# Kernel tuning notes

Hardware: AMD Instinct MI355X
Metric: run time of the kernel (lower is better)

The kernel has to match this reference:

```python
import jax, jax.numpy as jnp
import numpy as np

DEPTH = 3  # weights are SHARED across depth (same module object repeated in ModuleList)


def prelu(x, a):
    # nn.PReLU() with a single shared slope parameter
    return jnp.where(x >= 0, x, a * x)


def conv1x1(x, w, b):
    # x: (N,C,H,W), w: (O,C), b: (O,)
    return jnp.einsum('nchw,oc->nohw', x, w) + b[None, :, None, None]


def conv3x3(x, w, b):
    # w: (O,I,3,3), padding=1 stride=1 -> SAME
    y = jax.lax.conv_general_dilated(x, w, (1, 1), 'SAME',
                                     dimension_numbers=('NCHW', 'OIHW', 'NCHW'))
    return y + b[None, :, None, None]


def _unit(x, w1, b1, a1, w2, b2, a2, w3, b3, a3, wc, bc):
    # NonLocalAttention
    e1 = prelu(conv1x1(x, w1, b1), a1)   # (N,C,H,W)
    e2 = prelu(conv1x1(x, w2, b2), a2)   # (N,C,H,W)
    asm = prelu(conv1x1(x, w3, b3), a3)  # (N,C,H,W)
    N, C, H, W = e1.shape
    q = e1.reshape(N, C, H * W).transpose(0, 2, 1)     # (N,HW,C)
    k = e2.reshape(N, C, H * W)                        # (N,C,HW)
    score = jax.nn.softmax(jnp.matmul(q, k), axis=2)   # (N,HW,HW)
    v = asm.reshape(N, C, H * W).transpose(0, 2, 1)    # (N,HW,C)
    att = jnp.matmul(score, v).transpose(0, 2, 1).reshape(N, C, H, W)
    # Conv2d(channel, channel, 3, 1, 1) + exact GELU
    return jax.nn.gelu(conv3x3(att, wc, bc), approximate=False)


def setup_inputs() -> dict:
    key = jax.random.key(0)
    ks = jax.random.split(key, 8)
    C = 128
    x = jax.random.normal(ks[0], (1, C, 96, 96), dtype=jnp.float32)
    s = 0.05
    inp = {
        'x': x,
        'w1': jax.random.normal(ks[1], (C, C), jnp.float32) * s,
        'b1': jnp.zeros((C,), jnp.float32),
        'a1': jnp.float32(0.25),
        'w2': jax.random.normal(ks[2], (C, C), jnp.float32) * s,
        'b2': jnp.zeros((C,), jnp.float32),
        'a2': jnp.float32(0.25),
        'w3': jax.random.normal(ks[3], (C, C), jnp.float32) * s,
        'b3': jnp.zeros((C,), jnp.float32),
        'a3': jnp.float32(0.25),
        'wc': jax.random.normal(ks[4], (C, C, 3, 3), jnp.float32) * s,
        'bc': jnp.zeros((C,), jnp.float32),
    }
    return inp


def reference(x, w1, b1, a1, w2, b2, a2, w3, b3, a3, wc, bc):
    res = x
    for _ in range(DEPTH):  # same (shared) weights each iteration, per original module
        res = _unit(res, w1, b1, a1, w2, b2, a2, w3, b3, a3, wc, bc)
    return x + res
```

## Files before the change

kernel.cpp:

```cpp
#include <hip/hip_runtime.h>

#define HWPX 9216
#define NCH  128

typedef float  f32x4  __attribute__((ext_vector_type(4)));
typedef __bf16 bf16x8 __attribute__((ext_vector_type(8)));

#define SWZ16(row) ((((row) & 7) ^ (((row) >> 3) << 1)) << 4)

#define DPP_RED(v, OP)                                                         \
  do {                                                                         \
    v = OP(v, __int_as_float(__builtin_amdgcn_update_dpp(                      \
               0, __float_as_int(v), 0xB1, 0xF, 0xF, true)));                  \
    v = OP(v, __int_as_float(__builtin_amdgcn_update_dpp(                      \
               0, __float_as_int(v), 0x4E, 0xF, 0xF, true)));                  \
    v = OP(v, __int_as_float(__builtin_amdgcn_update_dpp(                      \
               0, __float_as_int(v), 0x124, 0xF, 0xF, true)));                 \
    v = OP(v, __int_as_float(__builtin_amdgcn_update_dpp(                      \
               0, __float_as_int(v), 0x128, 0xF, 0xF, true)));                 \
  } while (0)
__device__ __forceinline__ float op_max(float a, float b) { return fmaxf(a, b); }
__device__ __forceinline__ float op_add(float a, float b) { return a + b; }

__global__ __launch_bounds__(256) void prep_kernel(
    const float* __restrict__ w1, const float* __restrict__ w2,
    const float* __restrict__ w3, const float* __restrict__ wc,
    const float* __restrict__ x,
    __bf16* __restrict__ Wb, __bf16* __restrict__ wck,
    __bf16* __restrict__ Xb) {
  int tid = blockIdx.x * 256 + threadIdx.x;
  int nt  = gridDim.x * 256;
  for (int idx = tid; idx < 3 * 16384; idx += nt) {
    int j = idx >> 14;
    const float* w = (j == 0) ? w1 : (j == 1 ? w2 : w3);
    Wb[idx] = (__bf16)w[idx & 16383];
  }
  for (int idx = tid; idx < 147456; idx += nt) {
    int k = idx % 9;
    int rest = idx / 9;
    int c = rest & 127, o = rest >> 7;
    wck[(k * 128 + o) * 128 + c] = (__bf16)wc[idx];
  }
  for (int idx = tid; idx < 128 * HWPX; idx += nt) {
    int c = idx / HWPX, p = idx - c * HWPX;
    Xb[p * 128 + c] = (__bf16)x[idx];
  }
}

__global__ __launch_bounds__(256) void conv1x1_qkv(
    const __bf16* __restrict__ Xb, const __bf16* __restrict__ Wb,
    const float* __restrict__ b1, const float* __restrict__ b2,
    const float* __restrict__ b3, const float* __restrict__ a1,
    const float* __restrict__ a2, const float* __restrict__ a3,
    __bf16* __restrict__ Q, __bf16* __restrict__ K, __bf16* __restrict__ Vt) {
  const int tid = threadIdx.x, lane = tid & 63, w = tid >> 6;
  const int l16 = lane & 15, hi = lane >> 4;
  const int p0 = blockIdx.x * 64;
  const int z  = blockIdx.y;

  bf16x8 af[4][4];
#pragma unroll
  for (int pxt = 0; pxt < 4; ++pxt)
#pragma unroll
    for (int kc = 0; kc < 4; ++kc)
      af[pxt][kc] = *(const bf16x8*)&Xb[(p0 + pxt * 16 + l16) * 128 + kc * 32 + hi * 8];

  const int obase = w * 96 + z * 16;
  const int j = obase >> 7;
  const int oo = (obase & 127) + l16;
  bf16x8 bfg[4];
#pragma unroll
  for (int kc = 0; kc < 4; ++kc)
    bfg[kc] = *(const bf16x8*)&Wb[(obase + l16) * 128 + kc * 32 + hi * 8];
  f32x4 acc[4];
#pragma unroll
  for (int pxt = 0; pxt < 4; ++pxt) acc[pxt] = (f32x4){0.f, 0.f, 0.f, 0.f};
#pragma unroll
  for (int kc = 0; kc < 4; ++kc)
#pragma unroll
    for (int pxt = 0; pxt < 4; ++pxt)
      acc[pxt] = __builtin_amdgcn_mfma_f32_16x16x32_bf16(af[pxt][kc], bfg[kc], acc[pxt], 0, 0, 0);

  const float* bp = (j == 0) ? b1 : (j == 1 ? b2 : b3);
  const float bias = bp[oo];
  const float* ap = (j == 0) ? a1 : (j == 1 ? a2 : a3);
  const float sl = ap[0];
#pragma unroll
  for (int pxt = 0; pxt < 4; ++pxt)
#pragma unroll
    for (int r = 0; r < 4; ++r) {
      float v = acc[pxt][r] + bias;
      v = (v >= 0.f) ? v : sl * v;
      int px = p0 + pxt * 16 + hi * 4 + r;
      if (j == 0)      Q[px * 128 + oo] = (__bf16)v;
      else if (j == 1) K[px * 128 + oo] = (__bf16)v;
      else             Vt[oo * HWPX + px] = (__bf16)v;
    }
}

__global__ __launch_bounds__(512) void flash_attn(
    const __bf16* __restrict__ Q, const __bf16* __restrict__ Kb,
    const __bf16* __restrict__ Vt, float* __restrict__ Opart,
    float* __restrict__ mOut, float* __restrict__ lOut, int nt) {
  __shared__ __align__(16) unsigned char smem[81920];
  const int tid  = threadIdx.x;
  const int lane = tid & 63;
  const int w    = tid >> 6;
  const int l16  = lane & 15;
  const int hi   = lane >> 4;
  const int ord  = blockIdx.y * 72 + blockIdx.x;
  const int nsp  = gridDim.y;
  const int split = ord % nsp;
  const int qb   = (ord / nsp) * 128;
  const int kt0  = split * nt;

  const __bf16* gsrc[4];
  unsigned loff[4];
  long gstep;
  if (w < 4) {
    gstep = 8192;
#pragma unroll
    for (int j = 0; j < 4; ++j) {
      int seg = w * 4 + j;
      int row = seg * 4 + (lane >> 4);
      int ch  = lane & 15;
      gsrc[j] = Kb + (size_t)(kt0 * 64 + row) * 128 + (ch ^ (row & 7)) * 8;
      loff[j] = seg * 1024;
    }
  } else {
    gstep = 64;
#pragma unroll
    for (int j = 0; j < 4; ++j) {
      int seg = (w - 4) * 4 + j;
      int d  = seg * 8 + (lane >> 3);
      int ch = lane & 7;
      gsrc[j] = Vt + (size_t)d * HWPX + kt0 * 64 + (ch ^ (d & 7)) * 8;
      loff[j] = 16384 + seg * 1024;
    }
  }

#define STAGE(BUF) do {                                                        \
  _Pragma("unroll")                                                            \
  for (int j = 0; j < 4; ++j) {                                                \
    __builtin_amdgcn_global_load_lds(                                          \
        (const __attribute__((address_space(1))) unsigned int*)gsrc[j],        \
        (__attribute__((address_space(3))) unsigned int*)(smem + (BUF) * 32768 \
                                                          + loff[j]),          \
        16, 0, 0);                                                             \
    gsrc[j] += gstep;                                                          \
  } } while (0)

  bf16x8 qf[4];
  const int qrow = qb + w * 16 + l16;
#pragma unroll
  for (int dc = 0; dc < 4; ++dc)
    qf[dc] = *(const bf16x8*)&Q[qrow * 128 + dc * 32 + hi * 8];

  f32x4 oacc[8];
#pragma unroll
  for (int dc = 0; dc < 8; ++dc) oacc[dc] = (f32x4){0.f, 0.f, 0.f, 0.f};
  float m[4], l[4];
#pragma unroll
  for (int r = 0; r < 4; ++r) { m[r] = -INFINITY; l[r] = 0.f; }

  const unsigned pbase = 65536 + w * 2048;

  STAGE(0);
  __syncthreads();

  int cur = 0;
  for (int it = 0; it < nt; ++it) {
    if (it + 1 < nt) STAGE(cur ^ 1);

    const unsigned kb0 = cur * 32768;
    f32x4 s[4];
    __builtin_amdgcn_s_setprio(1);
#pragma unroll
    for (int g = 0; g < 4; ++g) {
      s[g] = (f32x4){0.f, 0.f, 0.f, 0.f};
      int row = g * 16 + l16;
#pragma unroll
      for (int dc = 0; dc < 4; ++dc) {
        bf16x8 kf = *(const bf16x8*)&smem[kb0 + row * 256 +
                        ((dc * 64 + hi * 16) ^ ((row & 7) << 4))];
        s[g] = __builtin_amdgcn_mfma_f32_16x16x32_bf16(qf[dc], kf, s[g], 0, 0, 0);
      }
    }
    __builtin_amdgcn_s_setprio(0);

    float mx[4];
#pragma unroll
    for (int r = 0; r < 4; ++r) {
      mx[r] = fmaxf(fmaxf(s[0][r], s[1][r]), fmaxf(s[2][r], s[3][r]));
      DPP_RED(mx[r], op_max);
    }
    bool need = false;
#pragma unroll
    for (int r = 0; r < 4; ++r) need = need || (mx[r] > m[r] + 8.f);
    if (__any(need)) {
#pragma unroll
      for (int r = 0; r < 4; ++r) {
        float mn = fmaxf(m[r], mx[r]);
        float alpha = __expf(m[r] - mn);
        m[r] = mn;
        l[r] *= alpha;
#pragma unroll
        for (int dc = 0; dc < 8; ++dc) oacc[dc][r] *= alpha;
      }
    }
    float rs[4];
#pragma unroll
    for (int r = 0; r < 4; ++r) rs[r] = 0.f;
#pragma unroll
    for (int g = 0; g < 4; ++g)
#pragma unroll
      for (int r = 0; r < 4; ++r) {
        float p = __expf(s[g][r] - m[r]);
        s[g][r] = p;
        rs[r] += p;
      }
#pragma unroll
    for (int r = 0; r < 4; ++r) {
      DPP_RED(rs[r], op_add);
      l[r] += rs[r];
    }

#pragma unroll
    for (int g = 0; g < 4; ++g)
#pragma unroll
      for (int r = 0; r < 4; ++r) {
        int row = hi * 4 + r;
        *(__bf16*)&smem[pbase + row * 128 +
                        ((g * 32 + l16 * 2) ^ SWZ16(row))] = (__bf16)s[g][r];
      }
    bf16x8 pa[2];
#pragma unroll
    for (int kc = 0; kc < 2; ++kc)
      pa[kc] = *(const bf16x8*)&smem[pbase + l16 * 128 +
                   ((kc * 64 + hi * 16) ^ SWZ16(l16))];
    __builtin_amdgcn_s_setprio(1);
#pragma unroll
    for (int dc = 0; dc < 8; ++dc) {
#pragma unroll
      for (int kc = 0; kc < 2; ++kc) {
        int row = dc * 16 + l16;
        bf16x8 vf = *(const bf16x8*)&smem[kb0 + 16384 + row * 128 +
                        ((kc * 64 + hi * 16) ^ ((row & 7) << 4))];
        oacc[dc] = __builtin_amdgcn_mfma_f32_16x16x32_bf16(pa[kc], vf, oacc[dc], 0, 0, 0);
      }
    }
    __builtin_amdgcn_s_setprio(0);
    __syncthreads();
    cur ^= 1;
  }
#undef STAGE

  const int sbase = split * HWPX;
#pragma unroll
  for (int dc = 0; dc < 8; ++dc)
#pragma unroll
    for (int r = 0; r < 4; ++r) {
      int q = qb + w * 16 + hi * 4 + r;
      Opart[(size_t)(sbase + q) * 128 + dc * 16 + l16] = oacc[dc][r];
    }
  if (l16 == 0) {
#pragma unroll
    for (int r = 0; r < 4; ++r) {
      int q = qb + w * 16 + hi * 4 + r;
      mOut[sbase + q] = m[r];
      lOut[sbase + q] = l[r];
    }
  }
}

__global__ __launch_bounds__(256) void flash_combine(
    const float* __restrict__ Opart, const float* __restrict__ mArr,
    const float* __restrict__ lArr, float* __restrict__ att, int ksplit) {
  int idx = blockIdx.x * 256 + threadIdx.x;
  int q = idx >> 5, d4 = idx & 31;
  float M = -INFINITY;
  for (int i = 0; i < ksplit; ++i) M = fmaxf(M, mArr[i * HWPX + q]);
  float denom = 0.f;
  f32x4 acc = (f32x4){0.f, 0.f, 0.f, 0.f};
  for (int i = 0; i < ksplit; ++i) {
    float wi = __expf(mArr[i * HWPX + q] - M);
    denom += lArr[i * HWPX + q] * wi;
    f32x4 v = *(const f32x4*)&Opart[((size_t)i * HWPX + q) * 128 + d4 * 4];
#pragma unroll
    for (int e = 0; e < 4; ++e) acc[e] += wi * v[e];
  }
  float inv = 1.f / denom;
  f32x4 r;
#pragma unroll
  for (int e = 0; e < 4; ++e) r[e] = acc[e] * inv;
  *(f32x4*)&att[(size_t)q * 128 + d4 * 4] = r;
}

__global__ __launch_bounds__(256) void conv3x3_gelu(
    const float* __restrict__ att, const __bf16* __restrict__ wck,
    const float* __restrict__ bc, const float* __restrict__ resid,
    float* __restrict__ out, __bf16* __restrict__ xbo) {
  __shared__ __align__(16) unsigned char smem[26112];
  const int tid = threadIdx.x;
  const int y   = blockIdx.x / 3;
  const int x0  = (blockIdx.x % 3) * 32;
  const int lane = tid & 63, w = tid >> 6;
  const int l16 = lane & 15, hi = lane >> 4;

  for (int id = tid; id < 1632; id += 256) {
    int px = id >> 4, ch = id & 15;
    int hy = px / 34, hx = px - hy * 34;
    int gy = y + hy - 1, gx = x0 + hx - 1;
    bf16x8 v;
    if (gy >= 0 && gy < 96 && gx >= 0 && gx < 96) {
      const float* src = &att[(gy * 96 + gx) * 128 + ch * 8];
      f32x4 aa = *(const f32x4*)src;
      f32x4 bb = *(const f32x4*)(src + 4);
#pragma unroll
      for (int e = 0; e < 4; ++e) { v[e] = (__bf16)aa[e]; v[4 + e] = (__bf16)bb[e]; }
    } else {
#pragma unroll
      for (int e = 0; e < 8; ++e) v[e] = (__bf16)0.f;
    }
    *(bf16x8*)&smem[px * 256 + ((ch * 16) ^ ((px & 7) << 4))] = v;
  }
  __syncthreads();

  f32x4 acc[2][2];
#pragma unroll
  for (int ot = 0; ot < 2; ++ot) {
    int obase = w * 32 + ot * 16 + hi * 4;
#pragma unroll
    for (int pt = 0; pt < 2; ++pt)
#pragma unroll
      for (int r = 0; r < 4; ++r) acc[ot][pt][r] = bc[obase + r];
  }

  for (int tap = 0; tap < 9; ++tap) {
    int dy = tap / 3, dx = tap - dy * 3;
#pragma unroll
    for (int cc = 0; cc < 4; ++cc) {
      bf16x8 af[2];
#pragma unroll
      for (int ot = 0; ot < 2; ++ot)
        af[ot] = *(const bf16x8*)&wck[(tap * 128 + w * 32 + ot * 16 + l16) * 128 +
                                      cc * 32 + hi * 8];
#pragma unroll
      for (int pt = 0; pt < 2; ++pt) {
        int px = dy * 34 + pt * 16 + l16 + dx;
        bf16x8 bf = *(const bf16x8*)&smem[px * 256 +
                        ((cc * 64 + hi * 16) ^ ((px & 7) << 4))];
#pragma unroll
        for (int ot = 0; ot < 2; ++ot)
          acc[ot][pt] = __builtin_amdgcn_mfma_f32_16x16x32_bf16(af[ot], bf, acc[ot][pt], 0, 0, 0);
      }
    }
  }

  float ge[2][2][4];
#pragma unroll
  for (int ot = 0; ot < 2; ++ot)
#pragma unroll
    for (int pt = 0; pt < 2; ++pt)
#pragma unroll
      for (int r = 0; r < 4; ++r) {
        float v = acc[ot][pt][r];
        ge[ot][pt][r] = 0.5f * v * (1.f + erff(v * 0.70710678118654752f));
      }

  if (xbo) {
    __syncthreads();
#pragma unroll
    for (int ot = 0; ot < 2; ++ot)
#pragma unroll
      for (int pt = 0; pt < 2; ++pt)
#pragma unroll
        for (int r = 0; r < 4; ++r) {
          int o  = w * 32 + ot * 16 + hi * 4 + r;
          int pl = pt * 16 + l16;
          *(__bf16*)&smem[pl * 256 + ((o * 2) ^ ((pl & 7) << 4))] =
              (__bf16)ge[ot][pt][r];
        }
    __syncthreads();
    for (int id = tid; id < 512; id += 256) {
      int pl = id >> 4, ch = id & 15;
      bf16x8 v = *(const bf16x8*)&smem[pl * 256 + ((ch * 16) ^ ((pl & 7) << 4))];
      *(bf16x8*)&xbo[(size_t)(y * 96 + x0 + pl) * 128 + ch * 8] = v;
    }
  } else {
#pragma unroll
    for (int ot = 0; ot < 2; ++ot)
#pragma unroll
      for (int pt = 0; pt < 2; ++pt)
#pragma unroll
        for (int r = 0; r < 4; ++r) {
          int o  = w * 32 + ot * 16 + hi * 4 + r;
          int px = y * 96 + x0 + pt * 16 + l16;
          out[o * HWPX + px] = ge[ot][pt][r] + resid[o * HWPX + px];
        }
  }
}

extern "C" void kernel_launch(void* const* d_in, const int* in_sizes, int n_in,
                              void* d_out, int out_size, void* d_ws, size_t ws_size,
                              hipStream_t stream) {
  const float* x  = (const float*)d_in[0];
  const float* w1 = (const float*)d_in[1];
  const float* b1 = (const float*)d_in[2];
  const float* a1 = (const float*)d_in[3];
  const float* w2 = (const float*)d_in[4];
  const float* b2 = (const float*)d_in[5];
  const float* a2 = (const float*)d_in[6];
  const float* w3 = (const float*)d_in[7];
  const float* b3 = (const float*)d_in[8];
  const float* a3 = (const float*)d_in[9];
  const float* wc = (const float*)d_in[10];
  const float* bc = (const float*)d_in[11];
  float* out = (float*)d_out;

  char* ws = (char*)d_ws;
  float*  att = (float*)(ws + 0);
  __bf16* Qb  = (__bf16*)(ws + 4718592);
  __bf16* Kb  = (__bf16*)(ws + 7077888);
  __bf16* Vt  = (__bf16*)(ws + 9437184);
  __bf16* Xb  = (__bf16*)(ws + 11796480);
  __bf16* Wb  = (__bf16*)(ws + 14155776);
  __bf16* wck = (__bf16*)(ws + 14254080);
  const size_t base_end = 14548992;

  int ksplit = 1;
  if (ws_size >= base_end + 8ull * (4718592 + 2 * 36864)) ksplit = 8;
  else if (ws_size >= base_end + 4ull * (4718592 + 2 * 36864)) ksplit = 4;
  else if (ws_size >= base_end + 2ull * (4718592 + 2 * 36864)) ksplit = 2;
  float* Opart = (float*)(ws + base_end);
  float* mArr  = (float*)(ws + base_end + (size_t)ksplit * 4718592);
  float* lArr  = (float*)(ws + base_end + (size_t)ksplit * (4718592 + 36864));

  prep_kernel<<<576, 256, 0, stream>>>(w1, w2, w3, wc, x, Wb, wck, Xb);

  for (int u = 0; u < 3; ++u) {
    conv1x1_qkv<<<dim3(144, 6), 256, 0, stream>>>(Xb, Wb, b1, b2, b3, a1, a2, a3,
                                                  Qb, Kb, Vt);
    flash_attn<<<dim3(72, ksplit), 512, 0, stream>>>(
        Qb, Kb, Vt, Opart, mArr, lArr, 144 / ksplit);
    flash_combine<<<1152, 256, 0, stream>>>(Opart, mArr, lArr, att, ksplit);
    conv3x3_gelu<<<288, 256, 0, stream>>>(att, wck, bc,
                                          (u == 2) ? x : nullptr,
                                          (u == 2) ? out : nullptr,
                                          (u < 2) ? Xb : nullptr);
  }
}
```

Measured before the change: 476.0 us.

## Use exp2 softmax with MFMA row sums, bf16 attention output, split conv3x3 channels

Q is pre-scaled by log2(e) so the flash kernel can use exp2 directly. Per-row sums are now computed with extra MFMAs against a ones vector, which replaces the DPP add reductions. The combine kernel writes bf16 attention output, halving that traffic, and the conv3x3 kernel reads it directly without converting. Conv3x3 is split over two output-channel halves to double the grid. The trade-off is two extra MFMAs per tile, and the row sum is now taken over bf16-rounded probabilities.

Measured after the change: 441.0 us. 1.08x faster.

```diff
diff --git a/kernel.cpp b/kernel.cpp
--- a/kernel.cpp
+++ b/kernel.cpp
@@ -5,22 +5,21 @@
 
 typedef float  f32x4  __attribute__((ext_vector_type(4)));
 typedef __bf16 bf16x8 __attribute__((ext_vector_type(8)));
+typedef __bf16 bf16x4 __attribute__((ext_vector_type(4)));
 
 #define SWZ16(row) ((((row) & 7) ^ (((row) >> 3) << 1)) << 4)
 
-#define DPP_RED(v, OP)                                                         \
+#define DPP_MAX(v)                                                             \
   do {                                                                         \
-    v = OP(v, __int_as_float(__builtin_amdgcn_update_dpp(                      \
+    v = fmaxf(v, __int_as_float(__builtin_amdgcn_update_dpp(                   \
                0, __float_as_int(v), 0xB1, 0xF, 0xF, true)));                  \
-    v = OP(v, __int_as_float(__builtin_amdgcn_update_dpp(                      \
+    v = fmaxf(v, __int_as_float(__builtin_amdgcn_update_dpp(                   \
                0, __float_as_int(v), 0x4E, 0xF, 0xF, true)));                  \
-    v = OP(v, __int_as_float(__builtin_amdgcn_update_dpp(                      \
+    v = fmaxf(v, __int_as_float(__builtin_amdgcn_update_dpp(                   \
                0, __float_as_int(v), 0x124, 0xF, 0xF, true)));                 \
-    v = OP(v, __int_as_float(__builtin_amdgcn_update_dpp(                      \
+    v = fmaxf(v, __int_as_float(__builtin_amdgcn_update_dpp(                   \
                0, __float_as_int(v), 0x128, 0xF, 0xF, true)));                 \
   } while (0)
-__device__ __forceinline__ float op_max(float a, float b) { return fmaxf(a, b); }
-__device__ __forceinline__ float op_add(float a, float b) { return a + b; }
 
 __global__ __launch_bounds__(256) void prep_kernel(
     const float* __restrict__ w1, const float* __restrict__ w2,
@@ -92,7 +91,7 @@
       float v = acc[pxt][r] + bias;
       v = (v >= 0.f) ? v : sl * v;
       int px = p0 + pxt * 16 + hi * 4 + r;
-      if (j == 0)      Q[px * 128 + oo] = (__bf16)v;
+      if (j == 0)      Q[px * 128 + oo] = (__bf16)(v * 1.44269504088896f);
       else if (j == 1) K[px * 128 + oo] = (__bf16)v;
       else             Vt[oo * HWPX + px] = (__bf16)v;
     }
@@ -156,12 +155,17 @@
   for (int dc = 0; dc < 4; ++dc)
     qf[dc] = *(const bf16x8*)&Q[qrow * 128 + dc * 32 + hi * 8];
 
+  bf16x8 ones;
+#pragma unroll
+  for (int e = 0; e < 8; ++e) ones[e] = (__bf16)1.0f;
+
   f32x4 oacc[8];
+  f32x4 oacc_l = (f32x4){0.f, 0.f, 0.f, 0.f};
 #pragma unroll
   for (int dc = 0; dc < 8; ++dc) oacc[dc] = (f32x4){0.f, 0.f, 0.f, 0.f};
-  float m[4], l[4];
-#pragma unroll
-  for (int r = 0; r < 4; ++r) { m[r] = -INFINITY; l[r] = 0.f; }
+  float m[4];
+#pragma unroll
+  for (int r = 0; r < 4; ++r) m[r] = -INFINITY;
 
   const unsigned pbase = 65536 + w * 2048;
 
@@ -192,7 +196,7 @@
 #pragma unroll
     for (int r = 0; r < 4; ++r) {
       mx[r] = fmaxf(fmaxf(s[0][r], s[1][r]), fmaxf(s[2][r], s[3][r]));
-      DPP_RED(mx[r], op_max);
+      DPP_MAX(mx[r]);
     }
     bool need = false;
 #pragma unroll
@@ -201,37 +205,21 @@
 #pragma unroll
       for (int r = 0; r < 4; ++r) {
         float mn = fmaxf(m[r], mx[r]);
-        float alpha = __expf(m[r] - mn);
+        float alpha = __builtin_amdgcn_exp2f(m[r] - mn);
         m[r] = mn;
-        l[r] *= alpha;
+        oacc_l[r] *= alpha;
 #pragma unroll
         for (int dc = 0; dc < 8; ++dc) oacc[dc][r] *= alpha;
       }
     }
-    float rs[4];
-#pragma unroll
-    for (int r = 0; r < 4; ++r) rs[r] = 0.f;
-#pragma unroll
-    for (int g = 0; g < 4; ++g)
-#pragma unroll
-      for (int r = 0; r < 4; ++r) {
-        float p = __expf(s[g][r] - m[r]);
-        s[g][r] = p;
-        rs[r] += p;
-      }
-#pragma unroll
-    for (int r = 0; r < 4; ++r) {
-      DPP_RED(rs[r], op_add);
-      l[r] += rs[r];
-    }
-
 #pragma unroll
     for (int g = 0; g < 4; ++g)
 #pragma unroll
       for (int r = 0; r < 4; ++r) {
         int row = hi * 4 + r;
         *(__bf16*)&smem[pbase + row * 128 +
-                        ((g * 32 + l16 * 2) ^ SWZ16(row))] = (__bf16)s[g][r];
+                        ((g * 32 + l16 * 2) ^ SWZ16(row))] =
+            (__bf16)__builtin_amdgcn_exp2f(s[g][r] - m[r]);
       }
     bf16x8 pa[2];
 #pragma unroll
@@ -249,6 +237,8 @@
         oacc[dc] = __builtin_amdgcn_mfma_f32_16x16x32_bf16(pa[kc], vf, oacc[dc], 0, 0, 0);
       }
     }
+    oacc_l = __builtin_amdgcn_mfma_f32_16x16x32_bf16(pa[0], ones, oacc_l, 0, 0, 0);
+    oacc_l = __builtin_amdgcn_mfma_f32_16x16x32_bf16(pa[1], ones, oacc_l, 0, 0, 0);
     __builtin_amdgcn_s_setprio(0);
     __syncthreads();
     cur ^= 1;
@@ -268,14 +258,14 @@
     for (int r = 0; r < 4; ++r) {
       int q = qb + w * 16 + hi * 4 + r;
       mOut[sbase + q] = m[r];
-      lOut[sbase + q] = l[r];
+      lOut[sbase + q] = oacc_l[r];
     }
   }
 }
 
 __global__ __launch_bounds__(256) void flash_combine(
     const float* __restrict__ Opart, const float* __restrict__ mArr,
-    const float* __restrict__ lArr, float* __restrict__ att, int ksplit) {
+    const float* __restrict__ lArr, __bf16* __restrict__ attb, int ksplit) {
   int idx = blockIdx.x * 256 + threadIdx.x;
   int q = idx >> 5, d4 = idx & 31;
   float M = -INFINITY;
@@ -283,27 +273,28 @@
   float denom = 0.f;
   f32x4 acc = (f32x4){0.f, 0.f, 0.f, 0.f};
   for (int i = 0; i < ksplit; ++i) {
-    float wi = __expf(mArr[i * HWPX + q] - M);
+    float wi = __builtin_amdgcn_exp2f(mArr[i * HWPX + q] - M);
     denom += lArr[i * HWPX + q] * wi;
     f32x4 v = *(const f32x4*)&Opart[((size_t)i * HWPX + q) * 128 + d4 * 4];
 #pragma unroll
     for (int e = 0; e < 4; ++e) acc[e] += wi * v[e];
   }
   float inv = 1.f / denom;
-  f32x4 r;
-#pragma unroll
-  for (int e = 0; e < 4; ++e) r[e] = acc[e] * inv;
-  *(f32x4*)&att[(size_t)q * 128 + d4 * 4] = r;
+  bf16x4 r;
+#pragma unroll
+  for (int e = 0; e < 4; ++e) r[e] = (__bf16)(acc[e] * inv);
+  *(bf16x4*)&attb[(size_t)q * 128 + d4 * 4] = r;
 }
 
 __global__ __launch_bounds__(256) void conv3x3_gelu(
-    const float* __restrict__ att, const __bf16* __restrict__ wck,
+    const __bf16* __restrict__ attb, const __bf16* __restrict__ wck,
     const float* __restrict__ bc, const float* __restrict__ resid,
     float* __restrict__ out, __bf16* __restrict__ xbo) {
   __shared__ __align__(16) unsigned char smem[26112];
   const int tid = threadIdx.x;
   const int y   = blockIdx.x / 3;
   const int x0  = (blockIdx.x % 3) * 32;
+  const int oh  = blockIdx.y;
   const int lane = tid & 63, w = tid >> 6;
   const int l16 = lane & 15, hi = lane >> 4;
 
@@ -313,11 +304,7 @@
     int gy = y + hy - 1, gx = x0 + hx - 1;
     bf16x8 v;
     if (gy >= 0 && gy < 96 && gx >= 0 && gx < 96) {
-      const float* src = &att[(gy * 96 + gx) * 128 + ch * 8];
-      f32x4 aa = *(const f32x4*)src;
-      f32x4 bb = *(const f32x4*)(src + 4);
-#pragma unroll
-      for (int e = 0; e < 4; ++e) { v[e] = (__bf16)aa[e]; v[4 + e] = (__bf16)bb[e]; }
+      v = *(const bf16x8*)&attb[(size_t)(gy * 96 + gx) * 128 + ch * 8];
     } else {
 #pragma unroll
       for (int e = 0; e < 8; ++e) v[e] = (__bf16)0.f;
@@ -326,78 +313,64 @@
   }
   __syncthreads();
 
-  f32x4 acc[2][2];
-#pragma unroll
-  for (int ot = 0; ot < 2; ++ot) {
-    int obase = w * 32 + ot * 16 + hi * 4;
-#pragma unroll
-    for (int pt = 0; pt < 2; ++pt)
-#pragma unroll
-      for (int r = 0; r < 4; ++r) acc[ot][pt][r] = bc[obase + r];
-  }
+  const int ob = oh * 64 + w * 16;
+  f32x4 acc[2];
+#pragma unroll
+  for (int pt = 0; pt < 2; ++pt)
+#pragma unroll
+    for (int r = 0; r < 4; ++r) acc[pt][r] = bc[ob + hi * 4 + r];
 
   for (int tap = 0; tap < 9; ++tap) {
     int dy = tap / 3, dx = tap - dy * 3;
 #pragma unroll
     for (int cc = 0; cc < 4; ++cc) {
-      bf16x8 af[2];
-#pragma unroll
-      for (int ot = 0; ot < 2; ++ot)
-        af[ot] = *(const bf16x8*)&wck[(tap * 128 + w * 32 + ot * 16 + l16) * 128 +
-                                      cc * 32 + hi * 8];
+      bf16x8 af = *(const bf16x8*)&wck[(tap * 128 + ob + l16) * 128 +
+                                       cc * 32 + hi * 8];
 #pragma unroll
       for (int pt = 0; pt < 2; ++pt) {
         int px = dy * 34 + pt * 16 + l16 + dx;
         bf16x8 bf = *(const bf16x8*)&smem[px * 256 +
                         ((cc * 64 + hi * 16) ^ ((px & 7) << 4))];
-#pragma unroll
-        for (int ot = 0; ot < 2; ++ot)
-          acc[ot][pt] = __builtin_amdgcn_mfma_f32_16x16x32_bf16(af[ot], bf, acc[ot][pt], 0, 0, 0);
-      }
-    }
-  }
-
-  float ge[2][2][4];
-#pragma unroll
-  for (int ot = 0; ot < 2; ++ot)
-#pragma unroll
-    for (int pt = 0; pt < 2; ++pt)
-#pragma unroll
-      for (int r = 0; r < 4; ++r) {
-        float v = acc[ot][pt][r];
-        ge[ot][pt][r] = 0.5f * v * (1.f + erff(v * 0.70710678118654752f));
-      }
+        acc[pt] = __builtin_amdgcn_mfma_f32_16x16x32_bf16(af, bf, acc[pt], 0, 0, 0);
+      }
+    }
+  }
+
+  float ge[2][4];
+#pragma unroll
+  for (int pt = 0; pt < 2; ++pt)
+#pragma unroll
+    for (int r = 0; r < 4; ++r) {
+      float v = acc[pt][r];
+      ge[pt][r] = 0.5f * v * (1.f + erff(v * 0.70710678118654752f));
+    }
 
   if (xbo) {
     __syncthreads();
 #pragma unroll
-    for (int ot = 0; ot < 2; ++ot)
-#pragma unroll
-      for (int pt = 0; pt < 2; ++pt)
-#pragma unroll
-        for (int r = 0; r < 4; ++r) {
-          int o  = w * 32 + ot * 16 + hi * 4 + r;
-          int pl = pt * 16 + l16;
-          *(__bf16*)&smem[pl * 256 + ((o * 2) ^ ((pl & 7) << 4))] =
-              (__bf16)ge[ot][pt][r];
-        }
+    for (int pt = 0; pt < 2; ++pt)
+#pragma unroll
+      for (int r = 0; r < 4; ++r) {
+        int oc = w * 16 + hi * 4 + r;
+        int pl = pt * 16 + l16;
+        *(__bf16*)&smem[pl * 256 + ((oc * 2) ^ ((pl & 7) << 4))] =
+            (__bf16)ge[pt][r];
+      }
     __syncthreads();
-    for (int id = tid; id < 512; id += 256) {
-      int pl = id >> 4, ch = id & 15;
+    for (int id = tid; id < 256; id += 256) {
+      int pl = id >> 3, ch = id & 7;
       bf16x8 v = *(const bf16x8*)&smem[pl * 256 + ((ch * 16) ^ ((pl & 7) << 4))];
-      *(bf16x8*)&xbo[(size_t)(y * 96 + x0 + pl) * 128 + ch * 8] = v;
+      *(bf16x8*)&xbo[(size_t)(y * 96 + x0 + pl) * 128 + oh * 64 + ch * 8] = v;
     }
   } else {
 #pragma unroll
-    for (int ot = 0; ot < 2; ++ot)
-#pragma unroll
-      for (int pt = 0; pt < 2; ++pt)
-#pragma unroll
-        for (int r = 0; r < 4; ++r) {
-          int o  = w * 32 + ot * 16 + hi * 4 + r;
-          int px = y * 96 + x0 + pt * 16 + l16;
-          out[o * HWPX + px] = ge[ot][pt][r] + resid[o * HWPX + px];
-        }
+    for (int pt = 0; pt < 2; ++pt)
+#pragma unroll
+      for (int r = 0; r < 4; ++r) {
+        int o  = ob + hi * 4 + r;
+        int px = y * 96 + x0 + pt * 16 + l16;
+        out[o * HWPX + px] = ge[pt][r] + resid[o * HWPX + px];
+      }
   }
 }
 
@@ -419,14 +392,14 @@
   float* out = (float*)d_out;
 
   char* ws = (char*)d_ws;
-  float*  att = (float*)(ws + 0);
-  __bf16* Qb  = (__bf16*)(ws + 4718592);
-  __bf16* Kb  = (__bf16*)(ws + 7077888);
-  __bf16* Vt  = (__bf16*)(ws + 9437184);
-  __bf16* Xb  = (__bf16*)(ws + 11796480);
-  __bf16* Wb  = (__bf16*)(ws + 14155776);
-  __bf16* wck = (__bf16*)(ws + 14254080);
-  const size_t base_end = 14548992;
+  __bf16* attb = (__bf16*)(ws + 0);
+  __bf16* Qb  = (__bf16*)(ws + 2359296);
+  __bf16* Kb  = (__bf16*)(ws + 4718592);
+  __bf16* Vt  = (__bf16*)(ws + 7077888);
+  __bf16* Xb  = (__bf16*)(ws + 9437184);
+  __bf16* Wb  = (__bf16*)(ws + 11796480);
+  __bf16* wck = (__bf16*)(ws + 11894784);
+  const size_t base_end = 12189696;
 
   int ksplit = 1;
   if (ws_size >= base_end + 8ull * (4718592 + 2 * 36864)) ksplit = 8;
@@ -443,10 +416,10 @@
                                                   Qb, Kb, Vt);
     flash_attn<<<dim3(72, ksplit), 512, 0, stream>>>(
         Qb, Kb, Vt, Opart, mArr, lArr, 144 / ksplit);
-    flash_combine<<<1152, 256, 0, stream>>>(Opart, mArr, lArr, att, ksplit);
-    conv3x3_gelu<<<288, 256, 0, stream>>>(att, wck, bc,
-                                          (u == 2) ? x : nullptr,
-                                          (u == 2) ? out : nullptr,
-                                          (u < 2) ? Xb : nullptr);
-  }
-}
+    flash_combine<<<1152, 256, 0, stream>>>(Opart, mArr, lArr, attb, ksplit);
+    conv3x3_gelu<<<dim3(288, 2), 256, 0, stream>>>(attb, wck, bc,
+                                                   (u == 2) ? x : nullptr,
+                                                   (u == 2) ? out : nullptr,
+                                                   (u < 2) ? Xb : nullptr);
+  }
+}
```
